# Kernel optimization log

Hardware: AMD Instinct MI355X
Metric: run time of the kernel (lower is better)

The kernel has to match this reference:

```python
import jax, jax.numpy as jnp
import numpy as np

NUM_NODES = 10000
NUM_EDGES = 640000
GNN_IN = 128
EDGE_DIST_DIM = 4
MLP_HIDDEN = 256
MLP_OUT = 1


def setup_inputs() -> dict:
    key = jax.random.key(0)
    k1, k2, k3, k4, k5 = jax.random.split(key, 5)
    x = jax.random.normal(k1, (NUM_NODES, GNN_IN), dtype=jnp.float32)
    edge_index = jax.random.randint(k2, (NUM_EDGES, 2), 0, NUM_NODES, dtype=jnp.int64)
    edge_dist = jax.random.normal(k3, (NUM_EDGES, EDGE_DIST_DIM), dtype=jnp.float32)
    d_in = GNN_IN * 2 + EDGE_DIST_DIM
    # Kaiming-uniform-ish init like nn.Linear defaults
    w1 = jax.random.uniform(k4, (d_in, MLP_HIDDEN), dtype=jnp.float32,
                            minval=-1.0, maxval=1.0) / np.sqrt(d_in)
    b1 = jnp.zeros((MLP_HIDDEN,), dtype=jnp.float32)
    w2 = jax.random.uniform(k5, (MLP_HIDDEN, MLP_OUT), dtype=jnp.float32,
                            minval=-1.0, maxval=1.0) / np.sqrt(MLP_HIDDEN)
    b2 = jnp.zeros((MLP_OUT,), dtype=jnp.float32)
    return {"x": x, "edge_index": edge_index, "edge_dist": edge_dist,
            "w1": w1, "b1": b1, "w2": w2, "b2": b2}


def reference(x, edge_index, edge_dist, w1, b1, w2, b2):
    # edge_index: (num_edges, 2) -> transpose to (2, num_edges) as in forward()
    row = edge_index[:, 0]
    col = edge_index[:, 1]
    # gather node features for both endpoints, concat with edge distances
    edge_attr = jnp.concatenate([x[row], x[col], edge_dist], axis=1)  # (E, 2*gnn_in+edge_dist_dim)
    h = jax.nn.relu(edge_attr @ w1 + b1)  # (E, mlp_hidden)
    return jax.nn.sigmoid(h @ w2 + b2)    # (E, mlp_out)
```

## Files before the change

kernel.cpp:

```cpp
#include <hip/hip_runtime.h>
#include <hip/hip_fp16.h>

#define GNN_IN 128
#define HID 256

typedef _Float16 f16x2 __attribute__((ext_vector_type(2)));
struct __align__(8) h4v { f16x2 a, b; };

__device__ __forceinline__ float fdot2f(f16x2 a, f16x2 b, float c) {
#if __has_builtin(__builtin_amdgcn_fdot2)
    return __builtin_amdgcn_fdot2(a, b, c, false);
#else
    return fmaf((float)a.x, (float)b.x, fmaf((float)a.y, (float)b.y, c));
#endif
}

__device__ __forceinline__ f16x2 pkcvt(float x, float y) {
#if __has_builtin(__builtin_amdgcn_cvt_pkrtz)
    return __builtin_bit_cast(f16x2, __builtin_amdgcn_cvt_pkrtz(x, y));
#else
    f16x2 r; r.x = (_Float16)x; r.y = (_Float16)y; return r;
#endif
}

#define DPP_ADD(v, ctrl)                                                     \
    do {                                                                     \
        float _t = __builtin_bit_cast(                                       \
            float, __builtin_amdgcn_update_dpp(                              \
                       0, __builtin_bit_cast(int, v), ctrl, 0xf, 0xf, true));\
        (v) += _t;                                                           \
    } while (0)

__device__ __forceinline__ float dpp_sum64(float v) {
    DPP_ADD(v, 0x111);
    DPP_ADD(v, 0x112);
    DPP_ADD(v, 0x114);
    DPP_ADD(v, 0x118);
    DPP_ADD(v, 0x142);
    DPP_ADD(v, 0x143);
    return v;
}

__global__ void detect_kernel(const unsigned int* __restrict__ ei,
                              unsigned int* __restrict__ flag) {
    if (threadIdx.x == 0 && blockIdx.x == 0) {
        unsigned int v = 0;
        for (int i = 1; i < 256; i += 2) v |= ei[i];
        *flag = (v == 0u) ? 1u : 0u;
    }
}

__global__ void __launch_bounds__(256) node_gemm_fused(
    const float* __restrict__ x, const float* __restrict__ w1,
    __half* __restrict__ AB, int num_nodes) {
    __shared__ float xs[16][GNN_IN];
    const int tid = threadIdx.x;
    const int r0  = blockIdx.x * 16;

    for (int i = tid; i < 16 * GNN_IN / 4; i += 256) {
        const int rr = i >> 5;
        const int cc = (i & 31) << 2;
        const int r = min(r0 + rr, num_nodes - 1);
        *(float4*)&xs[rr][cc] = *(const float4*)(x + (size_t)r * GNN_IN + cc);
    }
    __syncthreads();

    float accA[16], accB[16];
#pragma unroll
    for (int r = 0; r < 16; ++r) { accA[r] = 0.f; accB[r] = 0.f; }

    const float* __restrict__ wA = w1 + tid;
    const float* __restrict__ wB = w1 + (size_t)GNN_IN * HID + tid;

    for (int k0 = 0; k0 < GNN_IN; k0 += 4) {
        float wa[4], wb[4];
#pragma unroll
        for (int kk = 0; kk < 4; ++kk) {
            wa[kk] = wA[(size_t)(k0 + kk) * HID];
            wb[kk] = wB[(size_t)(k0 + kk) * HID];
        }
#pragma unroll
        for (int r = 0; r < 16; ++r) {
            const float4 xv = *(const float4*)&xs[r][k0];
            accA[r] = fmaf(xv.x, wa[0], accA[r]);
            accA[r] = fmaf(xv.y, wa[1], accA[r]);
            accA[r] = fmaf(xv.z, wa[2], accA[r]);
            accA[r] = fmaf(xv.w, wa[3], accA[r]);
            accB[r] = fmaf(xv.x, wb[0], accB[r]);
            accB[r] = fmaf(xv.y, wb[1], accB[r]);
            accB[r] = fmaf(xv.z, wb[2], accB[r]);
            accB[r] = fmaf(xv.w, wb[3], accB[r]);
        }
    }

    __half* oA = AB + tid;
    __half* oB = AB + (size_t)num_nodes * HID + tid;
#pragma unroll
    for (int r = 0; r < 16; ++r) {
        if (r0 + r < num_nodes) {
            oA[(size_t)(r0 + r) * HID] = __float2half_rn(accA[r]);
            oB[(size_t)(r0 + r) * HID] = __float2half_rn(accB[r]);
        }
    }
}

__global__ void __launch_bounds__(256) edge_kernel_fp16(
    const __half* __restrict__ A, const __half* __restrict__ B,
    const void* __restrict__ ei, const float* __restrict__ ed,
    const float* __restrict__ w1, const float* __restrict__ b1,
    const float* __restrict__ w2, const float* __restrict__ b2,
    const unsigned int* __restrict__ flag,
    float* __restrict__ out, int num_edges) {
    const int lane   = threadIdx.x & 63;
    const int wave   = (blockIdx.x * blockDim.x + threadIdx.x) >> 6;
    const int nwaves = (gridDim.x * blockDim.x) >> 6;
    const int c0     = lane << 2;

    const float4 b1v = *(const float4*)(b1 + c0);
    float wt[4][4];
#pragma unroll
    for (int k = 0; k < 4; ++k)
        *(float4*)wt[k] = *(const float4*)(w1 + (size_t)(2 * GNN_IN + k) * HID + c0);
    const float4 w2f = *(const float4*)(w2 + c0);
    const f16x2  w2A = pkcvt(w2f.x, w2f.y);
    const f16x2  w2B = pkcvt(w2f.z, w2f.w);
    const float  b2v = b2[0];
    const int   is64 = __builtin_amdgcn_readfirstlane((int)(*flag));
    const f16x2 zero = {(_Float16)0.f, (_Float16)0.f};

    const int chunk = (((num_edges + nwaves - 1) / nwaves) + 3) & ~3;
    const int e0s = __builtin_amdgcn_readfirstlane(wave * chunk);
    const int e1s = __builtin_amdgcn_readfirstlane(min(num_edges, e0s + chunk));

    for (int es = e0s; es < e1s; es += 4) {
        int eid[4];
#pragma unroll
        for (int j = 0; j < 4; ++j) eid[j] = min(es + j, e1s - 1);

        int rr[4], cc[4];
        if (is64) {
#pragma unroll
            for (int j = 0; j < 4; ++j) {
                const int4 v = *(const int4*)((const char*)ei + (size_t)eid[j] * 16);
                rr[j] = v.x; cc[j] = v.z;
            }
        } else {
#pragma unroll
            for (int j = 0; j < 4; ++j) {
                const int2 v = *(const int2*)((const char*)ei + (size_t)eid[j] * 8);
                rr[j] = v.x; cc[j] = v.y;
            }
        }

        h4v av[4], bv[4];
        float4 edv[4];
#pragma unroll
        for (int j = 0; j < 4; ++j) {
            av[j]  = *(const h4v*)(A + (size_t)rr[j] * HID + c0);
            bv[j]  = *(const h4v*)(B + (size_t)cc[j] * HID + c0);
            edv[j] = *(const float4*)(ed + (size_t)eid[j] * 4);
        }

        float p[4];
#pragma unroll
        for (int j = 0; j < 4; ++j) {
            float c_[4] = {b1v.x, b1v.y, b1v.z, b1v.w};
            const float ep[4] = {edv[j].x, edv[j].y, edv[j].z, edv[j].w};
#pragma unroll
            for (int k = 0; k < 4; ++k)
#pragma unroll
                for (int q = 0; q < 4; ++q) c_[q] = fmaf(ep[k], wt[k][q], c_[q]);
            f16x2 h0 = (av[j].a + bv[j].a) + pkcvt(c_[0], c_[1]);
            f16x2 h1 = (av[j].b + bv[j].b) + pkcvt(c_[2], c_[3]);
            h0 = __builtin_elementwise_max(h0, zero);
            h1 = __builtin_elementwise_max(h1, zero);
            p[j] = fdot2f(h0, w2A, fdot2f(h1, w2B, 0.f));
        }

#pragma unroll
        for (int j = 0; j < 4; ++j) p[j] = dpp_sum64(p[j]);

        float s[4];
#pragma unroll
        for (int j = 0; j < 4; ++j) s[j] = 1.f / (1.f + __expf(-(p[j] + b2v)));

        if (lane == 63) {
            if (es + 3 < e1s) {
                *(float4*)(out + es) = make_float4(s[0], s[1], s[2], s[3]);
            } else {
#pragma unroll
                for (int j = 0; j < 4; ++j)
                    if (es + j < e1s) out[es + j] = s[j];
            }
        }
    }
}

__global__ void __launch_bounds__(256) edge_direct_kernel(
    const float* __restrict__ x, const void* __restrict__ ei,
    const float* __restrict__ ed, const float* __restrict__ w1,
    const float* __restrict__ b1, const float* __restrict__ w2,
    const float* __restrict__ b2, const unsigned int* __restrict__ flag,
    float* __restrict__ out, int num_edges, int num_nodes) {
    const int lane   = threadIdx.x & 63;
    const int wave   = (blockIdx.x * blockDim.x + threadIdx.x) >> 6;
    const int nwaves = (gridDim.x * blockDim.x) >> 6;
    const int c0     = lane << 2;

    const float4 w2v = *(const float4*)(w2 + c0);
    const float4 b1v = *(const float4*)(b1 + c0);
    float wt[4][4];
#pragma unroll
    for (int k = 0; k < 4; ++k)
        *(float4*)wt[k] = *(const float4*)(w1 + (size_t)(2 * GNN_IN + k) * HID + c0);
    const float b2v  = b2[0];
    const int   is64 = flag ? (int)(*flag) : 0;

    const float* w2p = (const float*)&w2v;
    const float* b1p = (const float*)&b1v;

    const int chunk = (num_edges + nwaves - 1) / nwaves;
    const int e0 = wave * chunk;
    const int e1 = min(num_edges, e0 + chunk);

    for (int e = e0; e < e1; ++e) {
        int row, col;
        if (is64) {
            const int4 v = ((const int4*)ei)[e];
            row = v.x; col = v.z;
        } else {
            const int2 v = ((const int2*)ei)[e];
            row = v.x; col = v.y;
        }
        row = min(max(row, 0), num_nodes - 1);
        col = min(max(col, 0), num_nodes - 1);

        const float4 edv = *(const float4*)(ed + (size_t)e * 4);
        const float* edp = (const float*)&edv;

        float h4[4];
#pragma unroll
        for (int jj = 0; jj < 4; ++jj) {
            float h = b1p[jj];
#pragma unroll
            for (int k = 0; k < 4; ++k) h = fmaf(edp[k], wt[k][jj], h);
            h4[jj] = h;
        }
        const float* xr = x + (size_t)row * GNN_IN;
        const float* xc = x + (size_t)col * GNN_IN;
        for (int k = 0; k < GNN_IN; ++k) {
            const float xv = xr[k];
            const float4 wv = *(const float4*)(w1 + (size_t)k * HID + c0);
            h4[0] = fmaf(xv, wv.x, h4[0]); h4[1] = fmaf(xv, wv.y, h4[1]);
            h4[2] = fmaf(xv, wv.z, h4[2]); h4[3] = fmaf(xv, wv.w, h4[3]);
        }
        for (int k = 0; k < GNN_IN; ++k) {
            const float xv = xc[k];
            const float4 wv = *(const float4*)(w1 + (size_t)(GNN_IN + k) * HID + c0);
            h4[0] = fmaf(xv, wv.x, h4[0]); h4[1] = fmaf(xv, wv.y, h4[1]);
            h4[2] = fmaf(xv, wv.z, h4[2]); h4[3] = fmaf(xv, wv.w, h4[3]);
        }
        float p = 0.f;
#pragma unroll
        for (int jj = 0; jj < 4; ++jj) {
            const float h = fmaxf(h4[jj], 0.f);
            p = fmaf(h, w2p[jj], p);
        }
#pragma unroll
        for (int off = 32; off >= 1; off >>= 1) p += __shfl_xor(p, off, 64);
        if (lane == 0) out[e] = 1.f / (1.f + __expf(-(p + b2v)));
    }
}

extern "C" void kernel_launch(void* const* d_in, const int* in_sizes, int n_in,
                              void* d_out, int out_size, void* d_ws, size_t ws_size,
                              hipStream_t stream) {
    const float* x  = (const float*)d_in[0];
    const void*  ei = d_in[1];
    const float* ed = (const float*)d_in[2];
    const float* w1 = (const float*)d_in[3];
    const float* b1 = (const float*)d_in[4];
    const float* w2 = (const float*)d_in[5];
    const float* b2 = (const float*)d_in[6];
    float* out = (float*)d_out;

    const int num_nodes = in_sizes[0] / GNN_IN;
    const int num_edges = in_sizes[1] / 2;

    unsigned int* flag = nullptr;
    if (ws_size >= 16) {
        flag = (unsigned int*)d_ws;
        detect_kernel<<<1, 64, 0, stream>>>((const unsigned int*)ei, flag);
    }

    const size_t need = 256 + (size_t)2 * num_nodes * HID * sizeof(__half);
    if (flag && ws_size >= need) {
        __half* A = (__half*)((char*)d_ws + 256);
        node_gemm_fused<<<(num_nodes + 15) / 16, 256, 0, stream>>>(
            x, w1, A, num_nodes);
        __half* Bp = A + (size_t)num_nodes * HID;
        edge_kernel_fp16<<<2048, 256, 0, stream>>>(A, Bp, ei, ed, w1, b1, w2, b2,
                                                   flag, out, num_edges);
    } else {
        edge_direct_kernel<<<4096, 256, 0, stream>>>(x, ei, ed, w1, b1, w2, b2,
                                                     flag, out, num_edges, num_nodes);
    }
}
```

Before: 114.3 us.

## Split hidden dimension across blocks with partial sums and separate combine

```diff
diff --git a/kernel.cpp b/kernel.cpp
--- a/kernel.cpp
+++ b/kernel.cpp
@@ -3,6 +3,8 @@
 
 #define GNN_IN 128
 #define HID 256
+#define NSPLIT 4
+#define SLICE 64
 
 typedef _Float16 f16x2 __attribute__((ext_vector_type(2)));
 struct __align__(8) h4v { f16x2 a, b; };
@@ -31,11 +33,16 @@
         (v) += _t;                                                           \
     } while (0)
 
-__device__ __forceinline__ float dpp_sum64(float v) {
+__device__ __forceinline__ float dpp_sum16(float v) {
     DPP_ADD(v, 0x111);
     DPP_ADD(v, 0x112);
     DPP_ADD(v, 0x114);
     DPP_ADD(v, 0x118);
+    return v;
+}
+
+__device__ __forceinline__ float dpp_sum64(float v) {
+    v = dpp_sum16(v);
     DPP_ADD(v, 0x142);
     DPP_ADD(v, 0x143);
     return v;
@@ -50,7 +57,20 @@
     }
 }
 
-__global__ void __launch_bounds__(256) node_gemm_fused(
+__global__ void __launch_bounds__(256) decode_kernel(
+    const void* __restrict__ ei, const unsigned int* __restrict__ flag,
+    int2* __restrict__ idx, int ne) {
+    const int e = blockIdx.x * 256 + threadIdx.x;
+    if (e >= ne) return;
+    if (*flag) {
+        const int4 v = *(const int4*)((const char*)ei + (size_t)e * 16);
+        idx[e] = make_int2(v.x, v.z);
+    } else {
+        idx[e] = ((const int2*)ei)[e];
+    }
+}
+
+__global__ void __launch_bounds__(256) node_gemm_c4(
     const float* __restrict__ x, const float* __restrict__ w1,
     __half* __restrict__ AB, int num_nodes) {
     __shared__ float xs[16][GNN_IN];
@@ -65,43 +85,125 @@
     }
     __syncthreads();
 
-    float accA[16], accB[16];
-#pragma unroll
-    for (int r = 0; r < 16; ++r) { accA[r] = 0.f; accB[r] = 0.f; }
-
-    const float* __restrict__ wA = w1 + tid;
-    const float* __restrict__ wB = w1 + (size_t)GNN_IN * HID + tid;
+    const int cq   = tid & 127;
+    const int rg   = tid >> 7;
+    const int col  = (cq & 63) << 2;
+    const int half = cq >> 6;
+    const float* __restrict__ w = w1 + (size_t)half * GNN_IN * HID + col;
+
+    float acc[8][4];
+#pragma unroll
+    for (int r = 0; r < 8; ++r)
+#pragma unroll
+        for (int c = 0; c < 4; ++c) acc[r][c] = 0.f;
 
     for (int k0 = 0; k0 < GNN_IN; k0 += 4) {
-        float wa[4], wb[4];
-#pragma unroll
-        for (int kk = 0; kk < 4; ++kk) {
-            wa[kk] = wA[(size_t)(k0 + kk) * HID];
-            wb[kk] = wB[(size_t)(k0 + kk) * HID];
-        }
-#pragma unroll
-        for (int r = 0; r < 16; ++r) {
-            const float4 xv = *(const float4*)&xs[r][k0];
-            accA[r] = fmaf(xv.x, wa[0], accA[r]);
-            accA[r] = fmaf(xv.y, wa[1], accA[r]);
-            accA[r] = fmaf(xv.z, wa[2], accA[r]);
-            accA[r] = fmaf(xv.w, wa[3], accA[r]);
-            accB[r] = fmaf(xv.x, wb[0], accB[r]);
-            accB[r] = fmaf(xv.y, wb[1], accB[r]);
-            accB[r] = fmaf(xv.z, wb[2], accB[r]);
-            accB[r] = fmaf(xv.w, wb[3], accB[r]);
-        }
-    }
-
-    __half* oA = AB + tid;
-    __half* oB = AB + (size_t)num_nodes * HID + tid;
-#pragma unroll
-    for (int r = 0; r < 16; ++r) {
-        if (r0 + r < num_nodes) {
-            oA[(size_t)(r0 + r) * HID] = __float2half_rn(accA[r]);
-            oB[(size_t)(r0 + r) * HID] = __float2half_rn(accB[r]);
-        }
-    }
+        float4 wv[4];
+#pragma unroll
+        for (int kk = 0; kk < 4; ++kk)
+            wv[kk] = *(const float4*)(w + (size_t)(k0 + kk) * HID);
+#pragma unroll
+        for (int r = 0; r < 8; ++r) {
+            const float4 xv = *(const float4*)&xs[rg * 8 + r][k0];
+            acc[r][0] = fmaf(xv.x, wv[0].x, acc[r][0]);
+            acc[r][1] = fmaf(xv.x, wv[0].y, acc[r][1]);
+            acc[r][2] = fmaf(xv.x, wv[0].z, acc[r][2]);
+            acc[r][3] = fmaf(xv.x, wv[0].w, acc[r][3]);
+            acc[r][0] = fmaf(xv.y, wv[1].x, acc[r][0]);
+            acc[r][1] = fmaf(xv.y, wv[1].y, acc[r][1]);
+            acc[r][2] = fmaf(xv.y, wv[1].z, acc[r][2]);
+            acc[r][3] = fmaf(xv.y, wv[1].w, acc[r][3]);
+            acc[r][0] = fmaf(xv.z, wv[2].x, acc[r][0]);
+            acc[r][1] = fmaf(xv.z, wv[2].y, acc[r][1]);
+            acc[r][2] = fmaf(xv.z, wv[2].z, acc[r][2]);
+            acc[r][3] = fmaf(xv.z, wv[2].w, acc[r][3]);
+            acc[r][0] = fmaf(xv.w, wv[3].x, acc[r][0]);
+            acc[r][1] = fmaf(xv.w, wv[3].y, acc[r][1]);
+            acc[r][2] = fmaf(xv.w, wv[3].z, acc[r][2]);
+            acc[r][3] = fmaf(xv.w, wv[3].w, acc[r][3]);
+        }
+    }
+
+    __half* o = AB + (size_t)half * num_nodes * HID + col;
+#pragma unroll
+    for (int r = 0; r < 8; ++r) {
+        const int rr = r0 + rg * 8 + r;
+        if (rr < num_nodes) {
+            h4v hv;
+            hv.a = pkcvt(acc[r][0], acc[r][1]);
+            hv.b = pkcvt(acc[r][2], acc[r][3]);
+            *(h4v*)(o + (size_t)rr * HID) = hv;
+        }
+    }
+}
+
+__global__ void __launch_bounds__(256) edge_split_kernel(
+    const __half* __restrict__ AB, const int2* __restrict__ idx,
+    const float* __restrict__ ed, const float* __restrict__ w1,
+    const float* __restrict__ b1, const float* __restrict__ w2,
+    float* __restrict__ partials, int num_edges, int num_nodes) {
+    const int tid   = threadIdx.x;
+    const int lane  = tid & 63;
+    const int bid   = blockIdx.x;
+    const int split = (bid & 7) >> 1;
+    const int wsi   = ((((bid >> 3) << 1) | (bid & 1)) << 2) | (tid >> 6);
+    const int nsw   = (gridDim.x >> 3) << 3;
+    const int j     = lane >> 4;
+    const int q     = lane & 15;
+    const int c     = split * SLICE + (q << 2);
+
+    const float4 b1v = *(const float4*)(b1 + c);
+    const float  b1a[4] = {b1v.x, b1v.y, b1v.z, b1v.w};
+    f16x2 wt01[4], wt23[4];
+#pragma unroll
+    for (int cc = 0; cc < 4; ++cc) {
+        wt01[cc] = pkcvt(w1[(size_t)(2 * GNN_IN + 0) * HID + c + cc],
+                         w1[(size_t)(2 * GNN_IN + 1) * HID + c + cc]);
+        wt23[cc] = pkcvt(w1[(size_t)(2 * GNN_IN + 2) * HID + c + cc],
+                         w1[(size_t)(2 * GNN_IN + 3) * HID + c + cc]);
+    }
+    const float4 w2f = *(const float4*)(w2 + c);
+    const f16x2  w2A = pkcvt(w2f.x, w2f.y);
+    const f16x2  w2B = pkcvt(w2f.z, w2f.w);
+    const f16x2 zero = {(_Float16)0.f, (_Float16)0.f};
+
+    const __half* __restrict__ A = AB;
+    const __half* __restrict__ B = AB + (size_t)num_nodes * HID;
+    const int ngroups = (num_edges + 3) >> 2;
+
+    for (int grp = wsi; grp < ngroups; grp += nsw) {
+        const int e = min(grp * 4 + j, num_edges - 1);
+        const int2 rc = idx[e];
+        const float4 edv = *(const float4*)(ed + (size_t)e * 4);
+        const h4v av = *(const h4v*)(A + (size_t)rc.x * HID + c);
+        const h4v bv = *(const h4v*)(B + (size_t)rc.y * HID + c);
+
+        const f16x2 e01 = pkcvt(edv.x, edv.y);
+        const f16x2 e23 = pkcvt(edv.z, edv.w);
+        float c_[4];
+#pragma unroll
+        for (int cc = 0; cc < 4; ++cc)
+            c_[cc] = fdot2f(e01, wt01[cc], fdot2f(e23, wt23[cc], b1a[cc]));
+
+        f16x2 h0 = (av.a + bv.a) + pkcvt(c_[0], c_[1]);
+        f16x2 h1 = (av.b + bv.b) + pkcvt(c_[2], c_[3]);
+        h0 = __builtin_elementwise_max(h0, zero);
+        h1 = __builtin_elementwise_max(h1, zero);
+        float p = fdot2f(h0, w2A, fdot2f(h1, w2B, 0.f));
+
+        p = dpp_sum16(p);
+        if (q == 15) partials[(size_t)split * num_edges + e] = p;
+    }
+}
+
+__global__ void __launch_bounds__(256) combine_kernel(
+    const float* __restrict__ partials, const float* __restrict__ b2,
+    float* __restrict__ out, int ne) {
+    const int e = blockIdx.x * 256 + threadIdx.x;
+    if (e >= ne) return;
+    const float p = partials[e] + partials[(size_t)ne + e] +
+                    partials[(size_t)2 * ne + e] + partials[(size_t)3 * ne + e];
+    out[e] = 1.f / (1.f + __expf(-(p + b2[0])));
 }
 
 __global__ void __launch_bounds__(256) edge_kernel_fp16(
@@ -135,62 +237,56 @@
     for (int es = e0s; es < e1s; es += 4) {
         int eid[4];
 #pragma unroll
-        for (int j = 0; j < 4; ++j) eid[j] = min(es + j, e1s - 1);
-
+        for (int jj = 0; jj < 4; ++jj) eid[jj] = min(es + jj, e1s - 1);
         int rr[4], cc[4];
         if (is64) {
 #pragma unroll
-            for (int j = 0; j < 4; ++j) {
-                const int4 v = *(const int4*)((const char*)ei + (size_t)eid[j] * 16);
-                rr[j] = v.x; cc[j] = v.z;
+            for (int jj = 0; jj < 4; ++jj) {
+                const int4 v = *(const int4*)((const char*)ei + (size_t)eid[jj] * 16);
+                rr[jj] = v.x; cc[jj] = v.z;
             }
         } else {
 #pragma unroll
-            for (int j = 0; j < 4; ++j) {
-                const int2 v = *(const int2*)((const char*)ei + (size_t)eid[j] * 8);
-                rr[j] = v.x; cc[j] = v.y;
+            for (int jj = 0; jj < 4; ++jj) {
+                const int2 v = *(const int2*)((const char*)ei + (size_t)eid[jj] * 8);
+                rr[jj] = v.x; cc[jj] = v.y;
             }
         }
-
         h4v av[4], bv[4];
         float4 edv[4];
 #pragma unroll
-        for (int j = 0; j < 4; ++j) {
-            av[j]  = *(const h4v*)(A + (size_t)rr[j] * HID + c0);
-            bv[j]  = *(const h4v*)(B + (size_t)cc[j] * HID + c0);
-            edv[j] = *(const float4*)(ed + (size_t)eid[j] * 4);
-        }
-
+        for (int jj = 0; jj < 4; ++jj) {
+            av[jj]  = *(const h4v*)(A + (size_t)rr[jj] * HID + c0);
+            bv[jj]  = *(const h4v*)(B + (size_t)cc[jj] * HID + c0);
+            edv[jj] = *(const float4*)(ed + (size_t)eid[jj] * 4);
+        }
         float p[4];
 #pragma unroll
-        for (int j = 0; j < 4; ++j) {
+        for (int jj = 0; jj < 4; ++jj) {
             float c_[4] = {b1v.x, b1v.y, b1v.z, b1v.w};
-            const float ep[4] = {edv[j].x, edv[j].y, edv[j].z, edv[j].w};
+            const float ep[4] = {edv[jj].x, edv[jj].y, edv[jj].z, edv[jj].w};
 #pragma unroll
             for (int k = 0; k < 4; ++k)
 #pragma unroll
-                for (int q = 0; q < 4; ++q) c_[q] = fmaf(ep[k], wt[k][q], c_[q]);
-            f16x2 h0 = (av[j].a + bv[j].a) + pkcvt(c_[0], c_[1]);
-            f16x2 h1 = (av[j].b + bv[j].b) + pkcvt(c_[2], c_[3]);
+                for (int qq = 0; qq < 4; ++qq) c_[qq] = fmaf(ep[k], wt[k][qq], c_[qq]);
+            f16x2 h0 = (av[jj].a + bv[jj].a) + pkcvt(c_[0], c_[1]);
+            f16x2 h1 = (av[jj].b + bv[jj].b) + pkcvt(c_[2], c_[3]);
             h0 = __builtin_elementwise_max(h0, zero);
             h1 = __builtin_elementwise_max(h1, zero);
-            p[j] = fdot2f(h0, w2A, fdot2f(h1, w2B, 0.f));
-        }
-
-#pragma unroll
-        for (int j = 0; j < 4; ++j) p[j] = dpp_sum64(p[j]);
-
+            p[jj] = fdot2f(h0, w2A, fdot2f(h1, w2B, 0.f));
+        }
+#pragma unroll
+        for (int jj = 0; jj < 4; ++jj) p[jj] = dpp_sum64(p[jj]);
         float s[4];
 #pragma unroll
-        for (int j = 0; j < 4; ++j) s[j] = 1.f / (1.f + __expf(-(p[j] + b2v)));
-
+        for (int jj = 0; jj < 4; ++jj) s[jj] = 1.f / (1.f + __expf(-(p[jj] + b2v)));
         if (lane == 63) {
             if (es + 3 < e1s) {
                 *(float4*)(out + es) = make_float4(s[0], s[1], s[2], s[3]);
             } else {
 #pragma unroll
-                for (int j = 0; j < 4; ++j)
-                    if (es + j < e1s) out[es + j] = s[j];
+                for (int jj = 0; jj < 4; ++jj)
+                    if (es + jj < e1s) out[es + jj] = s[jj];
             }
         }
     }
@@ -215,7 +311,6 @@
         *(float4*)wt[k] = *(const float4*)(w1 + (size_t)(2 * GNN_IN + k) * HID + c0);
     const float b2v  = b2[0];
     const int   is64 = flag ? (int)(*flag) : 0;
-
     const float* w2p = (const float*)&w2v;
     const float* b1p = (const float*)&b1v;
 
@@ -234,10 +329,8 @@
         }
         row = min(max(row, 0), num_nodes - 1);
         col = min(max(col, 0), num_nodes - 1);
-
         const float4 edv = *(const float4*)(ed + (size_t)e * 4);
         const float* edp = (const float*)&edv;
-
         float h4[4];
 #pragma unroll
         for (int jj = 0; jj < 4; ++jj) {
@@ -262,10 +355,7 @@
         }
         float p = 0.f;
 #pragma unroll
-        for (int jj = 0; jj < 4; ++jj) {
-            const float h = fmaxf(h4[jj], 0.f);
-            p = fmaf(h, w2p[jj], p);
-        }
+        for (int jj = 0; jj < 4; ++jj) p = fmaf(fmaxf(h4[jj], 0.f), w2p[jj], p);
 #pragma unroll
         for (int off = 32; off >= 1; off >>= 1) p += __shfl_xor(p, off, 64);
         if (lane == 0) out[e] = 1.f / (1.f + __expf(-(p + b2v)));
@@ -293,13 +383,31 @@
         detect_kernel<<<1, 64, 0, stream>>>((const unsigned int*)ei, flag);
     }
 
-    const size_t need = 256 + (size_t)2 * num_nodes * HID * sizeof(__half);
-    if (flag && ws_size >= need) {
-        __half* A = (__half*)((char*)d_ws + 256);
-        node_gemm_fused<<<(num_nodes + 15) / 16, 256, 0, stream>>>(
-            x, w1, A, num_nodes);
-        __half* Bp = A + (size_t)num_nodes * HID;
-        edge_kernel_fp16<<<2048, 256, 0, stream>>>(A, Bp, ei, ed, w1, b1, w2, b2,
+    const size_t ab_bytes   = (size_t)2 * num_nodes * HID * sizeof(__half);
+    const size_t idx_bytes  = (size_t)num_edges * sizeof(int2);
+    const size_t part_bytes = (size_t)NSPLIT * num_edges * sizeof(float);
+    const size_t need_split = 256 + ab_bytes + idx_bytes + part_bytes;
+    const size_t need_old   = 256 + ab_bytes;
+
+    if (flag && ws_size >= need_split) {
+        __half* AB      = (__half*)((char*)d_ws + 256);
+        int2*   idx     = (int2*)((char*)d_ws + 256 + ab_bytes);
+        float*  partial = (float*)((char*)d_ws + 256 + ab_bytes + idx_bytes);
+
+        decode_kernel<<<(num_edges + 255) / 256, 256, 0, stream>>>(ei, flag, idx,
+                                                                   num_edges);
+        node_gemm_c4<<<(num_nodes + 15) / 16, 256, 0, stream>>>(x, w1, AB,
+                                                                num_nodes);
+        edge_split_kernel<<<2048, 256, 0, stream>>>(AB, idx, ed, w1, b1, w2,
+                                                    partial, num_edges, num_nodes);
+        combine_kernel<<<(num_edges + 255) / 256, 256, 0, stream>>>(partial, b2,
+                                                                    out, num_edges);
+    } else if (flag && ws_size >= need_old) {
+        __half* AB = (__half*)((char*)d_ws + 256);
+        node_gemm_c4<<<(num_nodes + 15) / 16, 256, 0, stream>>>(x, w1, AB,
+                                                                num_nodes);
+        __half* Bp = AB + (size_t)num_nodes * HID;
+        edge_kernel_fp16<<<2048, 256, 0, stream>>>(AB, Bp, ei, ed, w1, b1, w2, b2,
                                                    flag, out, num_edges);
     } else {
         edge_direct_kernel<<<4096, 256, 0, stream>>>(x, ei, ed, w1, b1, w2, b2,
```

Result: slower. 126.3 us (+10.5%).
